# Optimization experiments

Measured on AMD Instinct MI355X. Metric: run time of the kernel, lower is better.

The kernel has to match this reference:

```python
import jax, jax.numpy as jnp
import numpy as np
from jax import lax

T, B, NI, NH = 512, 64, 512, 512
SIGMA = 0.01


def _rnn_scan(inputs, W_xh, W_hh, b_h, h0):
    # inputs: [T, B, NI]; precompute input projection as one big GEMM
    xw = jnp.einsum('tbi,ih->tbh', inputs, W_xh)  # [T, B, NH]

    def step(h, x):
        h = jnp.tanh(x + h @ W_hh + b_h)
        return h, h

    hT, hs = lax.scan(step, h0, xw)
    return hs, hT  # hs: [T, B, NH]


def setup_inputs() -> dict:
    key = jax.random.key(0)
    ks = jax.random.split(key, 5)
    inputs = jax.random.normal(ks[0], (T, B, NI), dtype=jnp.float32)
    W_xh_f = jax.random.normal(ks[1], (NI, NH), dtype=jnp.float32) * SIGMA
    W_hh_f = jax.random.normal(ks[2], (NH, NH), dtype=jnp.float32) * SIGMA
    b_h_f = jnp.zeros((NH,), dtype=jnp.float32)
    W_xh_b = jax.random.normal(ks[3], (NI, NH), dtype=jnp.float32) * SIGMA
    W_hh_b = jax.random.normal(ks[4], (NH, NH), dtype=jnp.float32) * SIGMA
    b_h_b = jnp.zeros((NH,), dtype=jnp.float32)
    return {"inputs": inputs, "W_xh_f": W_xh_f, "W_hh_f": W_hh_f, "b_h_f": b_h_f,
            "W_xh_b": W_xh_b, "W_hh_b": W_hh_b, "b_h_b": b_h_b}


def reference(inputs, W_xh_f, W_hh_f, b_h_f, W_xh_b, W_hh_b, b_h_b):
    h0 = jnp.zeros((inputs.shape[1], NH), dtype=inputs.dtype)
    f_outs, f_H = _rnn_scan(inputs, W_xh_f, W_hh_f, b_h_f, h0)
    b_outs_rev, b_H = _rnn_scan(inputs[::-1], W_xh_b, W_hh_b, b_h_b, h0)
    b_outs = b_outs_rev[::-1]  # align backward outputs with forward time order
    outputs = jnp.concatenate([f_outs, b_outs], axis=-1)  # [T, B, 2*NH]
    return outputs, f_H, b_H
```

## Files before the change

### kernel.cpp

```cpp
#include <hip/hip_runtime.h>
#include <hip/hip_bf16.h>


typedef __attribute__((ext_vector_type(8))) short short8;
typedef __attribute__((ext_vector_type(4))) float f32x4;
typedef __attribute__((ext_vector_type(4))) int   i32x4;

static __device__ __forceinline__ unsigned short f2bf(float f) {
  unsigned int u = __builtin_bit_cast(unsigned int, f);
  u = (u + 0x7fffu + ((u >> 16) & 1u)) >> 16;
  return (unsigned short)u;
}
static __device__ __forceinline__ float bf2f(unsigned short s) {
  return __builtin_bit_cast(float, ((unsigned int)s) << 16);
}
static __device__ __forceinline__ float tanh_cheap(float x) {
  float t = x * 2.8853900817779268f;
  float e;
  asm("v_exp_f32 %0, %1" : "=v"(e) : "v"(t));
  float den = e + 1.0f;
  float r;
  asm("v_rcp_f32 %0, %1" : "=v"(r) : "v"(den));
  return __builtin_fmaf(-2.0f, r, 1.0f);
}
static __device__ __forceinline__ void lds_barrier() {
  __builtin_amdgcn_sched_barrier(0);
  asm volatile("s_waitcnt lgkmcnt(0)" ::: "memory");
  __builtin_amdgcn_s_barrier();
  __builtin_amdgcn_sched_barrier(0);
}
static __device__ __forceinline__ unsigned int cvt_pk_bf16(float a, float b) {
  unsigned int d;
  asm("v_cvt_pk_bf16_f32 %0, %1, %2" : "=v"(d) : "v"(a), "v"(b));
  return d;
}

__global__ __launch_bounds__(256, 2) void xw_gemm(
    const float* __restrict__ inp,
    const float* __restrict__ Wf,
    const float* __restrict__ Wb,
    const float* __restrict__ bhf,
    const float* __restrict__ bhb,
    unsigned short* __restrict__ xwpf,
    unsigned short* __restrict__ xwpb) {
  __shared__ unsigned short As[64 * 40];
  __shared__ unsigned short Bfs[64 * 40];
  __shared__ unsigned short Bbs[64 * 40];
  const int tid = threadIdx.x;
  const int w = tid >> 6, l = tid & 63;
  const int lr = l & 15, lg = l >> 4;
  const int rbase = blockIdx.x * 64;
  const int nbase = blockIdx.y * 64;

  f32x4 accf[4], accb[4];
#pragma unroll
  for (int tn = 0; tn < 4; ++tn) { accf[tn] = (f32x4){0,0,0,0}; accb[tn] = (f32x4){0,0,0,0}; }

  for (int i = 0; i < 16; ++i) {
    const int k0 = i * 32;
    __syncthreads();
#pragma unroll
    for (int e = 0; e < 2; ++e) {
      int lin4 = tid + e * 256;
      int r = lin4 >> 3, c4 = (lin4 & 7) * 4;
      float4 v = *reinterpret_cast<const float4*>(&inp[(rbase + r) * 512 + k0 + c4]);
      unsigned short* dst = &As[r * 40 + c4];
      dst[0] = f2bf(v.x); dst[1] = f2bf(v.y); dst[2] = f2bf(v.z); dst[3] = f2bf(v.w);
    }
#pragma unroll
    for (int e = 0; e < 2; ++e) {
      int lin4 = tid + e * 256;
      int r = lin4 >> 4, c4 = (lin4 & 15) * 4;
      float4 vf = *reinterpret_cast<const float4*>(&Wf[(k0 + r) * 512 + nbase + c4]);
      float4 vb = *reinterpret_cast<const float4*>(&Wb[(k0 + r) * 512 + nbase + c4]);
      Bfs[(c4 + 0) * 40 + r] = f2bf(vf.x);
      Bfs[(c4 + 1) * 40 + r] = f2bf(vf.y);
      Bfs[(c4 + 2) * 40 + r] = f2bf(vf.z);
      Bfs[(c4 + 3) * 40 + r] = f2bf(vf.w);
      Bbs[(c4 + 0) * 40 + r] = f2bf(vb.x);
      Bbs[(c4 + 1) * 40 + r] = f2bf(vb.y);
      Bbs[(c4 + 2) * 40 + r] = f2bf(vb.z);
      Bbs[(c4 + 3) * 40 + r] = f2bf(vb.w);
    }
    __syncthreads();
    const int ar = w * 16 + lr;
    const int kg = lg * 8;
    short8 a = *reinterpret_cast<const short8*>(&As[ar * 40 + kg]);
#pragma unroll
    for (int tn = 0; tn < 4; ++tn) {
      const int bc = tn * 16 + lr;
      short8 bf = *reinterpret_cast<const short8*>(&Bfs[bc * 40 + kg]);
      short8 bb = *reinterpret_cast<const short8*>(&Bbs[bc * 40 + kg]);
      accf[tn] = __builtin_amdgcn_mfma_f32_16x16x32_bf16(a, bf, accf[tn], 0, 0, 0);
      accb[tn] = __builtin_amdgcn_mfma_f32_16x16x32_bf16(a, bb, accb[tn], 0, 0, 0);
    }
  }
  unsigned long long* pf = reinterpret_cast<unsigned long long*>(xwpf);
  unsigned long long* pb = reinterpret_cast<unsigned long long*>(xwpb);
  const int b64 = (((int)blockIdx.x * 4 + w) * 16 + (int)blockIdx.y * 2) * 128 +
                  (lg * 16 + lr) * 2;
#pragma unroll
  for (int tn = 0; tn < 4; ++tn) {
    const int colb = nbase + tn * 16 + lr;
    const float bfv = bhf[colb], bbv = bhb[colb];
    unsigned long long vf =
        (unsigned long long)cvt_pk_bf16(accf[tn][0] + bfv, accf[tn][1] + bfv)
      | ((unsigned long long)cvt_pk_bf16(accf[tn][2] + bfv, accf[tn][3] + bfv) << 32);
    unsigned long long vb =
        (unsigned long long)cvt_pk_bf16(accb[tn][0] + bbv, accb[tn][1] + bbv)
      | ((unsigned long long)cvt_pk_bf16(accb[tn][2] + bbv, accb[tn][3] + bbv) << 32);
    pf[b64 + (tn >> 1) * 128 + (tn & 1)] = vf;
    pb[b64 + (tn >> 1) * 128 + (tn & 1)] = vb;
  }
}

__global__ __launch_bounds__(1024) void birnn_scan(
    const float* __restrict__ Whf, const float* __restrict__ Whb,
    unsigned short* __restrict__ xwpf, unsigned short* __restrict__ xwpb,
    float* __restrict__ out) {
  const int bid = blockIdx.x;
  const int d  = bid >> 2;
  const int rg = bid & 3;
  const int tid = threadIdx.x;
  const int w = tid >> 6, l = tid & 63;
  const int lr = l & 15, lg = l >> 4;
  const int cbase = w * 32;
  const int rbase = rg * 16;

  const float* Wh = d ? Whb : Whf;
  unsigned short* xwp = d ? xwpb : xwpf;

  __shared__ __align__(16) signed char hq[2][8192];

  const float sW = 127.0f / 0.06f;
  i32x4 wq[2][8];
#pragma unroll
  for (int n = 0; n < 2; ++n) {
    const int col = cbase + n * 16 + lr;
#pragma unroll
    for (int kk = 0; kk < 8; ++kk) {
      i32x4 v;
#pragma unroll
      for (int dw = 0; dw < 4; ++dw) {
        unsigned int pack = 0;
#pragma unroll
        for (int jj = 0; jj < 4; ++jj) {
          const int k = kk * 64 + lg * 16 + dw * 4 + jj;
          float wv = Wh[k * 512 + col] * sW;
          wv = fminf(fmaxf(wv, -127.f), 127.f);
          int q = (int)rintf(wv);
          pack |= ((unsigned int)(q & 0xff)) << (8 * jj);
        }
        v[dw] = (int)pack;
      }
      wq[n][kk] = v;
    }
  }
  const float inv_s = 1.0f / (127.0f * sW);

  short8 xA, xB;
  {
    const int t0 = d ? 511 : 0;
    xA = *reinterpret_cast<const short8*>(
        xwp + (((t0 * 4 + rg) * 16 + w) << 9) + (l << 3));
  }
  {
    const int t1 = d ? 510 : 1;
    xB = *reinterpret_cast<const short8*>(
        xwp + (((t1 * 4 + rg) * 16 + w) << 9) + (l << 3));
  }

  uint4 HP;

#define EPI(N, ACC, U0, U1, FINAL_)                                           \
  {                                                                           \
    float h0_ = tanh_cheap(fmaf((float)(ACC)[0], inv_s, bf2f((unsigned short)X[(N)*4+0]))); \
    float h1_ = tanh_cheap(fmaf((float)(ACC)[1], inv_s, bf2f((unsigned short)X[(N)*4+1]))); \
    float h2_ = tanh_cheap(fmaf((float)(ACC)[2], inv_s, bf2f((unsigned short)X[(N)*4+2]))); \
    float h3_ = tanh_cheap(fmaf((float)(ACC)[3], inv_s, bf2f((unsigned short)X[(N)*4+3]))); \
    signed char* hd_ = &hq[buf_][(w * 2 + (N)) * 256 + lg * 64 + lr];         \
    hd_[0]  = (signed char)(int)rintf(h0_ * 127.f);                           \
    hd_[16] = (signed char)(int)rintf(h1_ * 127.f);                           \
    hd_[32] = (signed char)(int)rintf(h2_ * 127.f);                           \
    hd_[48] = (signed char)(int)rintf(h3_ * 127.f);                           \
    U0 = cvt_pk_bf16(h0_, h1_);                                               \
    U1 = cvt_pk_bf16(h2_, h3_);                                               \
    if (FINAL_) {                                                             \
      float* fo_ = out + 33554432 + d * 32768 + (rbase + lg * 4) * 512 +      \
                   cbase + (N) * 16 + lr;                                     \
      fo_[0] = h0_; fo_[512] = h1_; fo_[1024] = h2_; fo_[1536] = h3_;         \
    }                                                                         \
  }

#define STEP(S, XARG, FINAL_)                                                 \
  do {                                                                        \
    const int s_ = (S);                                                       \
    const int t_ = d ? (511 - s_) : s_;                                       \
    const int buf_ = s_ & 1;                                                  \
    const int pb_ = (s_ - 1) & 1;                                             \
    short8& X = (XARG);                                                       \
    {              \
      const int tp_ = d ? (t_ + 1) : (t_ - 1);                                \
      unsigned short* pw_ = xwp + (((tp_ * 4 + rg) * 16 + w) << 9) + (l << 3);\
      *reinterpret_cast<uint4*>(pw_) = HP;                                    \
    }                                                                         \
    i32x4 acc0 = (i32x4){0,0,0,0}, acc1 = (i32x4){0,0,0,0};                   \
    __builtin_amdgcn_s_setprio(1);                                            \
    {                        \
      const signed char* hb_ = &hq[pb_][lg * 256 + lr * 16];                  \
      i32x4 a0 = *(const i32x4*)(hb_ + 0);                                    \
      i32x4 a1 = *(const i32x4*)(hb_ + 1024);                                 \
      i32x4 a2 = *(const i32x4*)(hb_ + 2048);                                 \
      i32x4 a3 = *(const i32x4*)(hb_ + 3072);                                 \
      acc0 = __builtin_amdgcn_mfma_i32_16x16x64_i8(a0, wq[0][0], acc0, 0, 0, 0); \
      acc1 = __builtin_amdgcn_mfma_i32_16x16x64_i8(a0, wq[1][0], acc1, 0, 0, 0); \
      acc0 = __builtin_amdgcn_mfma_i32_16x16x64_i8(a1, wq[0][1], acc0, 0, 0, 0); \
      acc1 = __builtin_amdgcn_mfma_i32_16x16x64_i8(a1, wq[1][1], acc1, 0, 0, 0); \
      acc0 = __builtin_amdgcn_mfma_i32_16x16x64_i8(a2, wq[0][2], acc0, 0, 0, 0); \
      acc1 = __builtin_amdgcn_mfma_i32_16x16x64_i8(a2, wq[1][2], acc1, 0, 0, 0); \
      acc0 = __builtin_amdgcn_mfma_i32_16x16x64_i8(a3, wq[0][3], acc0, 0, 0, 0); \
      acc1 = __builtin_amdgcn_mfma_i32_16x16x64_i8(a3, wq[1][3], acc1, 0, 0, 0); \
    }                                                                         \
    {                                              \
      const signed char* hb_ = &hq[pb_][(16 + lg) * 256 + lr * 16];           \
      i32x4 a0 = *(const i32x4*)(hb_ + 0);                                    \
      i32x4 a1 = *(const i32x4*)(hb_ + 1024);                                 \
      i32x4 a2 = *(const i32x4*)(hb_ + 2048);                                 \
      i32x4 a3 = *(const i32x4*)(hb_ + 3072);                                 \
      acc0 = __builtin_amdgcn_mfma_i32_16x16x64_i8(a0, wq[0][4], acc0, 0, 0, 0); \
      acc1 = __builtin_amdgcn_mfma_i32_16x16x64_i8(a0, wq[1][4], acc1, 0, 0, 0); \
      acc0 = __builtin_amdgcn_mfma_i32_16x16x64_i8(a1, wq[0][5], acc0, 0, 0, 0); \
      acc1 = __builtin_amdgcn_mfma_i32_16x16x64_i8(a1, wq[1][5], acc1, 0, 0, 0); \
      acc0 = __builtin_amdgcn_mfma_i32_16x16x64_i8(a2, wq[0][6], acc0, 0, 0, 0); \
      acc1 = __builtin_amdgcn_mfma_i32_16x16x64_i8(a2, wq[1][6], acc1, 0, 0, 0); \
      acc0 = __builtin_amdgcn_mfma_i32_16x16x64_i8(a3, wq[0][7], acc0, 0, 0, 0); \
      acc1 = __builtin_amdgcn_mfma_i32_16x16x64_i8(a3, wq[1][7], acc1, 0, 0, 0); \
    }                                                                         \
    __builtin_amdgcn_s_setprio(0);                                            \
    EPI(0, acc0, HP.x, HP.y, FINAL_);                                         \
    EPI(1, acc1, HP.z, HP.w, FINAL_);                                         \
    {                                    \
      const int tp2_ = d ? (t_ - 2) : (t_ + 2);                               \
      X = *reinterpret_cast<const short8*>(                                   \
          xwp + (((tp2_ * 4 + rg) * 16 + w) << 9) + (l << 3));                \
    }                                                                         \
    lds_barrier();                                                            \
  } while (0)

  {
    const int t_ = d ? 511 : 0;
    const int buf_ = 0;
    short8& X = xA;
    i32x4 z_ = (i32x4){0, 0, 0, 0};
    EPI(0, z_, HP.x, HP.y, 0);
    EPI(1, z_, HP.z, HP.w, 0);
    {
      const int tp2_ = d ? (t_ - 2) : (t_ + 2);
      xA = *reinterpret_cast<const short8*>(
          xwp + (((tp2_ * 4 + rg) * 16 + w) << 9) + (l << 3));
    }
    lds_barrier();
  }

  for (int ss = 0; ss < 255; ++ss) {
    STEP(1 + 2 * ss, xB, 0);
    STEP(2 + 2 * ss, xA, 0);
  }
  STEP(511, xB, 1);

  {
    const int tl_ = d ? 0 : 511;
    unsigned short* pw_ = xwp + (((tl_ * 4 + rg) * 16 + w) << 9) + (l << 3);
    *reinterpret_cast<uint4*>(pw_) = HP;
  }
#undef STEP
#undef EPI
}

__global__ __launch_bounds__(1024) void expand_out(
    const unsigned short* __restrict__ xwpf,
    const unsigned short* __restrict__ xwpb,
    float* __restrict__ out) {
  const int g = blockIdx.x * 1024 + threadIdx.x;
  const int flat = g * 4;
  const int row = flat >> 10;
  const int c   = flat & 1023;
  const int t = row >> 6, b = row & 63;
  const int d = c >> 9, col = c & 511;
  const unsigned short* buf = d ? xwpb : xwpf;
  const int lr0 = col & 15;
  const int base = ((t * 4 + (b >> 4)) * 16 + (col >> 5)) * 512 +
                   (((b >> 2) & 3) * 16) * 8 + ((col >> 4) & 1) * 4 + (b & 3);
  float4 v;
  v.x = bf2f(buf[base + (lr0 + 0) * 8]);
  v.y = bf2f(buf[base + (lr0 + 1) * 8]);
  v.z = bf2f(buf[base + (lr0 + 2) * 8]);
  v.w = bf2f(buf[base + (lr0 + 3) * 8]);
  *reinterpret_cast<float4*>(out + flat) = v;
}

extern "C" void kernel_launch(void* const* d_in, const int* in_sizes, int n_in,
                              void* d_out, int out_size, void* d_ws, size_t ws_size,
                              hipStream_t stream) {
  (void)in_sizes; (void)n_in; (void)out_size; (void)ws_size;
  const float* inputs = (const float*)d_in[0];
  const float* W_xh_f = (const float*)d_in[1];
  const float* W_hh_f = (const float*)d_in[2];
  const float* b_h_f  = (const float*)d_in[3];
  const float* W_xh_b = (const float*)d_in[4];
  const float* W_hh_b = (const float*)d_in[5];
  const float* b_h_b  = (const float*)d_in[6];

  unsigned short* xwpf = (unsigned short*)d_ws;
  unsigned short* xwpb = xwpf + 16777216 + 65536;

  dim3 g1(512, 8), b1(256);
  xw_gemm<<<g1, b1, 0, stream>>>(inputs, W_xh_f, W_xh_b, b_h_f, b_h_b, xwpf, xwpb);

  birnn_scan<<<dim3(8), dim3(1024), 0, stream>>>(
      W_hh_f, W_hh_b, xwpf, xwpb, (float*)d_out);

  expand_out<<<dim3(8192), dim3(1024), 0, stream>>>(xwpf, xwpb, (float*)d_out);
}
```

Before: 843.9 us.

## Replace per-step block barrier with LDS flag-based producer/consumer sync and 4-deep buffers

Each scan step previously ended with a full workgroup barrier. Now each wave publishes per-wave write and read progress counters in LDS and spins (with s_sleep) only until every wave's counter reaches the needed step. The hidden-state buffer grows from 2 to 4 slots so faster waves can run ahead, which lets waves drift instead of lockstepping. The cost is polling traffic on LDS, extra waitcnts, and the risk of memory-ordering bugs because the release/acquire relies on volatile LDS accesses.

```diff
diff --git a/kernel.cpp b/kernel.cpp
--- a/kernel.cpp
+++ b/kernel.cpp
@@ -22,12 +22,6 @@
   float r;
   asm("v_rcp_f32 %0, %1" : "=v"(r) : "v"(den));
   return __builtin_fmaf(-2.0f, r, 1.0f);
-}
-static __device__ __forceinline__ void lds_barrier() {
-  __builtin_amdgcn_sched_barrier(0);
-  asm volatile("s_waitcnt lgkmcnt(0)" ::: "memory");
-  __builtin_amdgcn_s_barrier();
-  __builtin_amdgcn_sched_barrier(0);
 }
 static __device__ __forceinline__ unsigned int cvt_pk_bf16(float a, float b) {
   unsigned int d;
@@ -130,7 +124,11 @@
   const float* Wh = d ? Whb : Whf;
   unsigned short* xwp = d ? xwpb : xwpf;
 
-  __shared__ __align__(16) signed char hq[2][8192];
+  __shared__ __align__(16) signed char hq[4][8192];
+  __shared__ int wpos[16];
+  __shared__ int rpos[16];
+  if (tid < 16) { wpos[tid] = 0; rpos[tid] = 0; }
+  __syncthreads();
 
   const float sW = 127.0f / 0.06f;
   i32x4 wq[2][8];
@@ -196,10 +194,17 @@
   do {                                                                        \
     const int s_ = (S);                                                       \
     const int t_ = d ? (511 - s_) : s_;                                       \
-    const int buf_ = s_ & 1;                                                  \
-    const int pb_ = (s_ - 1) & 1;                                             \
+    const int buf_ = s_ & 3;                                                  \
+    const int pb_ = (s_ - 1) & 3;                                             \
     short8& X = (XARG);                                                       \
-    {              \
+                            \
+    while (true) {                                                            \
+      int v_ = *(volatile int*)&wpos[l & 15];                                 \
+      if (__ballot(v_ >= s_) == ~0ull) break;                                 \
+      __builtin_amdgcn_s_sleep(1);                                            \
+    }                                                                         \
+    asm volatile("" ::: "memory");                                            \
+    {                                    \
       const int tp_ = d ? (t_ + 1) : (t_ - 1);                                \
       unsigned short* pw_ = xwp + (((tp_ * 4 + rg) * 16 + w) << 9) + (l << 3);\
       *reinterpret_cast<uint4*>(pw_) = HP;                                    \
@@ -237,14 +242,28 @@
       acc1 = __builtin_amdgcn_mfma_i32_16x16x64_i8(a3, wq[1][7], acc1, 0, 0, 0); \
     }                                                                         \
     __builtin_amdgcn_s_setprio(0);                                            \
+                   \
+    asm volatile("s_waitcnt lgkmcnt(0)" ::: "memory");                        \
+    if (l == 0) *(volatile int*)&rpos[w] = s_;                                \
+         \
+    if (s_ >= 4) {                                                            \
+      while (true) {                                                          \
+        int v_ = *(volatile int*)&rpos[l & 15];                               \
+        if (__ballot(v_ >= s_ - 3) == ~0ull) break;                           \
+        __builtin_amdgcn_s_sleep(1);                                          \
+      }                                                                       \
+      asm volatile("" ::: "memory");                                          \
+    }                                                                         \
     EPI(0, acc0, HP.x, HP.y, FINAL_);                                         \
     EPI(1, acc1, HP.z, HP.w, FINAL_);                                         \
+                              \
+    asm volatile("s_waitcnt lgkmcnt(0)" ::: "memory");                        \
+    if (l == 0) *(volatile int*)&wpos[w] = s_ + 1;                            \
     {                                    \
       const int tp2_ = d ? (t_ - 2) : (t_ + 2);                               \
       X = *reinterpret_cast<const short8*>(                                   \
           xwp + (((tp2_ * 4 + rg) * 16 + w) << 9) + (l << 3));                \
     }                                                                         \
-    lds_barrier();                                                            \
   } while (0)
 
   {
@@ -254,12 +273,13 @@
     i32x4 z_ = (i32x4){0, 0, 0, 0};
     EPI(0, z_, HP.x, HP.y, 0);
     EPI(1, z_, HP.z, HP.w, 0);
+    asm volatile("s_waitcnt lgkmcnt(0)" ::: "memory");
+    if (l == 0) *(volatile int*)&wpos[w] = 1;
     {
       const int tp2_ = d ? (t_ - 2) : (t_ + 2);
       xA = *reinterpret_cast<const short8*>(
           xwp + (((tp2_ * 4 + rg) * 16 + w) << 9) + (l << 3));
     }
-    lds_barrier();
   }
 
   for (int ss = 0; ss < 255; ++ss) {
```

After: 968.9 us. 14.8% more time.
